# Performance work log

Hardware: AMD Instinct MI355X
Metric: run time of the kernel (lower is better)

## Reference

```python
import jax, jax.numpy as jnp
import numpy as np

B, S, D, H = 4, 2048, 1024, 16
DH = D // H  # 64, head_embed_dim


def setup_inputs() -> dict:
    key = jax.random.key(0)
    ks = jax.random.split(key, 12)
    scale = 1.0 / np.sqrt(D)
    inp = {
        "query": jax.random.normal(ks[0], (B, S, D), jnp.float32),
        "key": jax.random.normal(ks[1], (B, S, D), jnp.float32),
        "value": jax.random.normal(ks[2], (B, S, D), jnp.float32),
        "key_padding_mask": jax.random.randint(ks[3], (B, S), 0, 2).astype(bool),
        # Linear params stored as [in, out] (math-equivalent to torch's [out,in].T)
        "Wq": jax.random.normal(ks[4], (D, H * DH), jnp.float32) * scale,
        "bq": jnp.zeros((H * DH,), jnp.float32),
        "Wk": jax.random.normal(ks[5], (D, H * DH), jnp.float32) * scale,
        "bk": jnp.zeros((H * DH,), jnp.float32),
        "Wv": jax.random.normal(ks[6], (D, H * DH), jnp.float32) * scale,
        "bv": jnp.zeros((H * DH,), jnp.float32),
        "Wo": jax.random.normal(ks[7], (H * DH, D), jnp.float32) * scale,
        "bo": jnp.zeros((D,), jnp.float32),
    }
    return inp


def reference(query, key, value, key_padding_mask, Wq, bq, Wk, bk, Wv, bv, Wo, bo):
    b, nq, _ = query.shape
    nk = key.shape[-2]
    # QKV projections -> [B, H, S, DH]
    q = (query @ Wq + bq).reshape(b, nq, H, DH).transpose(0, 2, 1, 3)
    k = (key @ Wk + bk).reshape(b, nk, H, DH).transpose(0, 2, 1, 3)
    v = (value @ Wv + bv).reshape(b, nk, H, DH).transpose(0, 2, 1, 3)
    # scaled dot-product scores [B, H, Sq, Sk]
    scores = jnp.einsum("bhqd,bhkd->bhqk", q, k) / np.sqrt(DH)
    # key_padding_mask broadcast over heads and query positions; True = masked
    mask = key_padding_mask[:, None, None, :]
    scores = jnp.where(mask, -jnp.inf, scores)
    w = jax.nn.softmax(scores, axis=-1)
    attn = jnp.einsum("bhqk,bhkd->bhqd", w, v)
    attn = attn.transpose(0, 2, 1, 3).reshape(b, nq, H * DH)
    return attn @ Wo + bo
```

## Files before the change

kernel.cpp:

```cpp
#include <hip/hip_runtime.h>
#include <hip/hip_bf16.h>

#define Bc 4
#define Sc 2048
#define Dc 1024
#define Hc 16
#define DHc 64

typedef unsigned short u16;
typedef unsigned int u32;
typedef __attribute__((ext_vector_type(8))) short bfrag;
typedef __attribute__((ext_vector_type(4))) float f32x4;

#define SCALE_Q 0.18033688011112042f

#if __has_builtin(__builtin_amdgcn_exp2f)
#define EXP2(x) __builtin_amdgcn_exp2f(x)
#else
#define EXP2(x) exp2f(x)
#endif

#if __has_builtin(__builtin_amdgcn_mfma_f32_16x16x16bf16_1k)
#define HAVE_M16 1
typedef __attribute__((ext_vector_type(4))) short bfrag4;
union FB4 { bfrag4 f; u32 w[2]; };
#endif

__device__ __forceinline__ u16 f2bf(float f) {
  u32 u = __float_as_uint(f);
  return (u16)((u + 0x7fffu + ((u >> 16) & 1u)) >> 16);
}
__device__ __forceinline__ float bf2f(u16 h) { return __uint_as_float(((u32)h) << 16); }

__device__ __forceinline__ u32 pkbf(float a, float b) {
  union { __hip_bfloat162 h; u32 u; } c;
  c.h = __float22bfloat162_rn(make_float2(a, b));
  return c.u;
}

union FB { bfrag f; u32 w[4]; };

__device__ __forceinline__ void gl_lds16(const u16* g, u16* l) {
  __builtin_amdgcn_global_load_lds(
      (const __attribute__((address_space(1))) unsigned int*)g,
      (__attribute__((address_space(3))) unsigned int*)l, 16, 0, 0);
}

__global__ __launch_bounds__(256) void prep_kernel(
    const void* __restrict__ qsrc, const void* __restrict__ mask,
    const void* __restrict__ bq, const void* __restrict__ bk,
    const void* __restrict__ bv, const void* __restrict__ bo,
    int* __restrict__ flags, float* __restrict__ maskf, float* __restrict__ biasf) {
  __shared__ int c_bf, c_ni, c_nf;
  const int tid = threadIdx.x;
  if (tid == 0) { c_bf = 0; c_ni = 0; c_nf = 0; }
  __syncthreads();
  u32 w = ((const u32*)qsrc)[tid];
  int e = (int)((w >> 7) & 0xffu);
  if (e >= 118 && e <= 130) atomicAdd(&c_bf, 1);
  int ni = 0, nf = 0;
  for (int i = tid; i < 2048; i += 256) {
    u32 v = ((const u32*)mask)[i];
    if (v > 1u) ni = 1;
    if (v != 0u && v != 0x3f800000u) nf = 1;
  }
  if (ni) atomicAdd(&c_ni, 1);
  if (nf) atomicAdd(&c_nf, 1);
  __syncthreads();
  const int isbf = (c_bf > 128) ? 1 : 0;
  const int layout = (c_ni == 0) ? 0 : ((c_nf == 0) ? 2 : 1);
  if (tid == 0) { flags[0] = isbf; flags[1] = layout; }
  for (int i = tid; i < Bc * Sc; i += 256) {
    int mv;
    if (layout == 0) mv = ((const int*)mask)[i];
    else if (layout == 1) mv = (int)((const unsigned char*)mask)[i];
    else mv = (((const u32*)mask)[i] != 0u) ? 1 : 0;
    maskf[i] = mv ? -1e30f : 0.0f;
  }
  const void* bs[4] = {bq, bk, bv, bo};
  for (int j = 0; j < 4; ++j) {
    const void* bp = bs[j];
    float sc = (j == 0) ? SCALE_Q : 1.0f;
    for (int i = tid; i < Dc; i += 256)
      biasf[j * Dc + i] = (isbf ? bf2f(((const u16*)bp)[i]) : ((const float*)bp)[i]) * sc;
  }
}

__global__ __launch_bounds__(256) void cvt3(
    const void* __restrict__ s0, const void* __restrict__ s1, const void* __restrict__ s2,
    u16* __restrict__ d0, u16* __restrict__ d1, u16* __restrict__ d2,
    const int* __restrict__ flags) {
  const void* s = blockIdx.y == 0 ? s0 : (blockIdx.y == 1 ? s1 : s2);
  u16* d = blockIdx.y == 0 ? d0 : (blockIdx.y == 1 ? d1 : d2);
  size_t e = ((size_t)blockIdx.x * 256 + threadIdx.x) * 8;
  if (flags[0]) {
    *(uint4*)(d + e) = *(const uint4*)((const u16*)s + e);
  } else {
    const float* p = (const float*)s + e;
    float4 f0 = *(const float4*)p, f1 = *(const float4*)(p + 4);
    uint4 st;
    st.x = pkbf(f0.x, f0.y); st.y = pkbf(f0.z, f0.w);
    st.z = pkbf(f1.x, f1.y); st.w = pkbf(f1.z, f1.w);
    *(uint4*)(d + e) = st;
  }
}

__global__ __launch_bounds__(256) void transpose_all(
    const void* __restrict__ W0, const void* __restrict__ W1,
    const void* __restrict__ W2, const void* __restrict__ W3,
    u16* __restrict__ D0, u16* __restrict__ D1, u16* __restrict__ D2,
    u16* __restrict__ D3, const int* __restrict__ flags) {
  __shared__ short ts[64][72];
  const int z = blockIdx.z;
  const void* W = z == 0 ? W0 : (z == 1 ? W1 : (z == 2 ? W2 : W3));
  u16* Wt = z == 0 ? D0 : (z == 1 ? D1 : (z == 2 ? D2 : D3));
  const float scale = (z == 0) ? SCALE_Q : 1.0f;
  const int r0 = blockIdx.y * 64, c0 = blockIdx.x * 64;
  const int isbf = flags[0];
  for (int i = 0; i < 2; ++i) {
    int ch = threadIdx.x + i * 256;
    int r = ch >> 3, c = (ch & 7) * 8;
    bfrag pk;
    if (isbf) {
      uint4 v = *(const uint4*)((const u16*)W + (size_t)(r0 + r) * Dc + c0 + c);
      const u16* pv = (const u16*)&v;
      for (int j = 0; j < 8; ++j) pk[j] = (short)f2bf(bf2f(pv[j]) * scale);
    } else {
      const float* p = (const float*)W + (size_t)(r0 + r) * Dc + c0 + c;
      float4 f0 = *(const float4*)p, f1 = *(const float4*)(p + 4);
      pk[0] = (short)f2bf(f0.x * scale); pk[1] = (short)f2bf(f0.y * scale);
      pk[2] = (short)f2bf(f0.z * scale); pk[3] = (short)f2bf(f0.w * scale);
      pk[4] = (short)f2bf(f1.x * scale); pk[5] = (short)f2bf(f1.y * scale);
      pk[6] = (short)f2bf(f1.z * scale); pk[7] = (short)f2bf(f1.w * scale);
    }
    *(bfrag*)(&ts[r][c]) = pk;
  }
  __syncthreads();
  for (int i = 0; i < 2; ++i) {
    int ch = threadIdx.x + i * 256;
    int n = ch >> 3, k = (ch & 7) * 8;
    u16 tmp[8] __attribute__((aligned(16)));
    for (int j = 0; j < 8; ++j) tmp[j] = (u16)ts[k + j][n];
    *(uint4*)(Wt + (size_t)(c0 + n) * Dc + r0 + k) = *(const uint4*)tmp;
  }
}

#define BM 128
#define BN 128
#define BK 32

#define GEMM_STAGE(bufI)                                                          \
  {                                                                               \
    gl_lds16(bgp0, &Bs[bufI][wave * 16][0]);                                      \
    gl_lds16(bgp1, &Bs[bufI][wave * 16 + 64][0]);                                 \
    bgp0 += BK; bgp1 += BK;                                                       \
    if (a_bf) {                                                                   \
      gl_lds16(agp0, &As[bufI][wave * 16][0]);                                    \
      gl_lds16(agp1, &As[bufI][wave * 16 + 64][0]);                               \
      agp0 += BK; agp1 += BK;                                                     \
    } else {                                                                      \
      for (int i_ = 0; i_ < 2; ++i_) {                                            \
        int ch_ = tid + i_ * 256;                                                 \
        int r_ = ch_ >> 2, kc_ = (ch_ & 3) * 8;                                   \
        const float* p_ = (const float*)Araw + (size_t)(bm0 + r_) * K + ksf + kc_;\
        float4 f0_ = *(const float4*)p_, f1_ = *(const float4*)(p_ + 4);          \
        uint4 st_;                                                                \
        st_.x = pkbf(f0_.x, f0_.y); st_.y = pkbf(f0_.z, f0_.w);                   \
        st_.z = pkbf(f1_.x, f1_.y); st_.w = pkbf(f1_.z, f1_.w);                   \
        *(uint4*)(&As[bufI][r_][kc_]) = st_;                                      \
      }                                                                           \
    }                                                                             \
    ksf += BK;                                                                    \
  }

__global__ __launch_bounds__(256) void gemm_bt(
    const void* __restrict__ Araw, const u16* __restrict__ Bt,
    const float* __restrict__ bias, void* __restrict__ Cout, u16* __restrict__ VtOut,
    const int* __restrict__ flags, int M, int N, int K,
    int a_mode , int c_mode ,
    int qkv ) {
  __shared__ __align__(16) u16 As[2][BM][BK];
  __shared__ __align__(16) u16 Bs[2][BN][BK];
  if (qkv) {
    const int z = blockIdx.z;
    Araw = (const void*)((const u16*)Araw + (size_t)z * Bc * Sc * Dc);
    Bt += (size_t)z * Dc * Dc;
    bias += z * Dc;
    if (z == 2) { c_mode = 2; Cout = (void*)VtOut; }
    else Cout = (void*)((u16*)Cout + (size_t)z * Bc * Sc * Dc);
  }
  const int tid = threadIdx.x;
  const int lane = tid & 63, wave = tid >> 6;
  const int lr = lane & 15, lq = lane >> 4;
  const int ntiles = N >> 7;
  const int band = (M >> 7) >> 3;
  const int L = blockIdx.x;
  const int mt = (L & 7) * band + ((L >> 3) / ntiles);
  const int nt = (L >> 3) % ntiles;
  const int bm0 = mt * BM, bn0 = nt * BN;
  const int wm = (wave >> 1) * 64, wn = (wave & 1) * 64;
  const int a_bf = a_mode ? 1 : flags[0];
  const int srow = lane >> 2;
  const int schunk = lane & 3;
  const u16* bgp0 = Bt + (size_t)(bn0 + wave * 16 + srow) * K + schunk * 8;
  const u16* bgp1 = bgp0 + (size_t)64 * K;
  const u16* agp0 = (const u16*)Araw + (size_t)(bm0 + wave * 16 + srow) * K + schunk * 8;
  const u16* agp1 = agp0 + (size_t)64 * K;
  int ksf = 0;
  f32x4 acc[4][4] = {};
  GEMM_STAGE(0);
  __syncthreads();
  const int NIT = K / BK;
#pragma unroll 2
  for (int it = 0; it < NIT; ++it) {
    const int p = it & 1;
    if (it + 1 < NIT) { GEMM_STAGE(p ^ 1); }
    bfrag af[4], bf[4];
    for (int mi = 0; mi < 4; ++mi) af[mi] = *(const bfrag*)(&As[p][wm + mi * 16 + lr][lq * 8]);
    for (int nj = 0; nj < 4; ++nj) bf[nj] = *(const bfrag*)(&Bs[p][wn + nj * 16 + lr][lq * 8]);
    for (int mi = 0; mi < 4; ++mi)
      for (int nj = 0; nj < 4; ++nj)
        acc[mi][nj] = __builtin_amdgcn_mfma_f32_16x16x32_bf16(af[mi], bf[nj], acc[mi][nj], 0, 0, 0);
    __syncthreads();
  }
  float bcol[4];
  for (int nj = 0; nj < 4; ++nj) bcol[nj] = bias[bn0 + wn + nj * 16 + lr];
  if (c_mode == 2) {
    u16* VT = (u16*)Cout;
    for (int mi = 0; mi < 4; ++mi)
      for (int nj = 0; nj < 4; ++nj) {
        int row = bm0 + wm + mi * 16 + lq * 4;
        int col = bn0 + wn + nj * 16 + lr;
        float v0 = acc[mi][nj][0] + bcol[nj], v1 = acc[mi][nj][1] + bcol[nj];
        float v2 = acc[mi][nj][2] + bcol[nj], v3 = acc[mi][nj][3] + bcol[nj];
        uint2 st;
        st.x = (u32)f2bf(v0) | ((u32)f2bf(v1) << 16);
        st.y = (u32)f2bf(v2) | ((u32)f2bf(v3) << 16);
        size_t drow = (size_t)((row >> 11) * Hc + (col >> 6)) * DHc + (col & 63);
        *(uint2*)(VT + drow * Sc + (row & (Sc - 1))) = st;
      }
  } else {
    const int outbf = (c_mode == 0) ? 1 : flags[0];
    for (int mi = 0; mi < 4; ++mi)
      for (int r = 0; r < 4; ++r) {
        int row = bm0 + wm + mi * 16 + lq * 4 + r;
        for (int nj = 0; nj < 4; ++nj) {
          int col = bn0 + wn + nj * 16 + lr;
          float v = acc[mi][nj][r] + bcol[nj];
          if (outbf) ((u16*)Cout)[(size_t)row * N + col] = f2bf(v);
          else ((float*)Cout)[(size_t)row * N + col] = v;
        }
      }
  }
}

__global__ __launch_bounds__(256) void attn_kernel(
    const u16* __restrict__ Q, const u16* __restrict__ K,
    const u16* __restrict__ Vt, const float* __restrict__ maskf,
    u16* __restrict__ Aout) {
  __shared__ __align__(16) u16 Ks[2][64][64];
  __shared__ __align__(16) u16 Vts[2][64][64];
  __shared__ float maskL[Sc];
  const int tid = threadIdx.x;
  const int lane = tid & 63, wave = tid >> 6;
  const int lr = lane & 15, lq = lane >> 4;
  const int bh = blockIdx.x;
  const int b = bh >> 4, h = bh & 15;
  const int q0 = blockIdx.y * 128;
  const int wq = wave * 32;
  const int rr0 = wave * 16 + (lane >> 3);
  const int rr1 = rr0 + 8;
  const int cc = lane & 7;
  const u16* kg0 = K + (size_t)(b * Sc + rr0) * Dc + h * DHc + ((cc ^ (rr0 & 7)) * 8);
  const u16* kg1 = K + (size_t)(b * Sc + rr1) * Dc + h * DHc + ((cc ^ (rr1 & 7)) * 8);
  const u16* vg0 = Vt + (size_t)((b * Hc + h) * DHc + rr0) * Sc + ((cc ^ (rr0 & 7)) * 8);
  const u16* vg1 = Vt + (size_t)((b * Hc + h) * DHc + rr1) * Sc + ((cc ^ (rr1 & 7)) * 8);
#define ATTN_STAGE(bufI)                                      \
  {                                                           \
    gl_lds16(kg0, &Ks[bufI][wave * 16][0]);                   \
    gl_lds16(kg1, &Ks[bufI][wave * 16 + 8][0]);               \
    gl_lds16(vg0, &Vts[bufI][wave * 16][0]);                  \
    gl_lds16(vg1, &Vts[bufI][wave * 16 + 8][0]);              \
    kg0 += (size_t)64 * Dc; kg1 += (size_t)64 * Dc;           \
    vg0 += 64; vg1 += 64;                                     \
  }
  bfrag qf[2][2];
  for (int mi = 0; mi < 2; ++mi)
    for (int ks = 0; ks < 2; ++ks)
      qf[mi][ks] = *(const bfrag*)(Q + (size_t)(b * Sc + q0 + wq + mi * 16 + lr) * Dc +
                                   h * DHc + ks * 32 + lq * 8);
  f32x4 oacc[2][4] = {};
  f32x4 oext[2] = {};
#ifdef HAVE_M16
  FB4 ones;
  ones.w[0] = 0x3F803F80u; ones.w[1] = 0x3F803F80u;
#else
  FB ones;
  ones.w[0] = 0x3F803F80u; ones.w[1] = 0x3F803F80u; ones.w[2] = 0x3F803F80u; ones.w[3] = 0x3F803F80u;
#endif
  ATTN_STAGE(0);
  {
    const float4* ms = (const float4*)(maskf + b * Sc);
    for (int i = tid; i < Sc / 4; i += 256) ((float4*)maskL)[i] = ms[i];
  }
  __syncthreads();
  const int lrx = lr & 7;
#pragma unroll 2
  for (int kt = 0; kt < Sc / 64; ++kt) {
    const int p = kt & 1;
    if (kt + 1 < Sc / 64) { ATTN_STAGE(p ^ 1); }
    f32x4 sacc[2][4];
    for (int nk = 0; nk < 4; ++nk) {
      f32x4 mk = *(const f32x4*)(&maskL[kt * 64 + nk * 16 + lq * 4]);
      sacc[0][nk] = mk;
      sacc[1][nk] = mk;
    }
    for (int nk = 0; nk < 4; ++nk) {
      const int kr = nk * 16 + lr;
      bfrag kf0 = *(const bfrag*)(&Ks[p][kr][(lq ^ lrx) * 8]);
      bfrag kf1 = *(const bfrag*)(&Ks[p][kr][((4 + lq) ^ lrx) * 8]);
      for (int mi = 0; mi < 2; ++mi) {
        sacc[mi][nk] = __builtin_amdgcn_mfma_f32_16x16x32_bf16(kf0, qf[mi][0], sacc[mi][nk], 0, 0, 0);
        sacc[mi][nk] = __builtin_amdgcn_mfma_f32_16x16x32_bf16(kf1, qf[mi][1], sacc[mi][nk], 0, 0, 0);
      }
    }
    for (int nk = 0; nk < 4; ++nk) {
      u32 pw[2][2];
      for (int mi = 0; mi < 2; ++mi) {
        float p0 = EXP2(sacc[mi][nk][0]);
        float p1 = EXP2(sacc[mi][nk][1]);
        float p2 = EXP2(sacc[mi][nk][2]);
        float p3 = EXP2(sacc[mi][nk][3]);
        pw[mi][0] = pkbf(p0, p1);
        pw[mi][1] = pkbf(p2, p3);
      }
      const int vchunk = (2 * nk + (lq >> 1));
      const int voff = (lq & 1) * 4;
#ifdef HAVE_M16
      FB4 pb0, pb1;
      pb0.w[0] = pw[0][0]; pb0.w[1] = pw[0][1];
      pb1.w[0] = pw[1][0]; pb1.w[1] = pw[1][1];
      oext[0] = __builtin_amdgcn_mfma_f32_16x16x16bf16_1k(ones.f, pb0.f, oext[0], 0, 0, 0);
      oext[1] = __builtin_amdgcn_mfma_f32_16x16x16bf16_1k(ones.f, pb1.f, oext[1], 0, 0, 0);
      for (int nd = 0; nd < 4; ++nd) {
        const int dr = nd * 16 + lr;
        FB4 vb;
        *(uint2*)&vb.w[0] = *(const uint2*)(&Vts[p][dr][(vchunk ^ lrx) * 8 + voff]);
        oacc[0][nd] = __builtin_amdgcn_mfma_f32_16x16x16bf16_1k(vb.f, pb0.f, oacc[0][nd], 0, 0, 0);
        oacc[1][nd] = __builtin_amdgcn_mfma_f32_16x16x16bf16_1k(vb.f, pb1.f, oacc[1][nd], 0, 0, 0);
      }
#else
      FB pb0, pb1;
      pb0.w[0] = pw[0][0]; pb0.w[1] = pw[0][1]; pb0.w[2] = 0; pb0.w[3] = 0;
      pb1.w[0] = pw[1][0]; pb1.w[1] = pw[1][1]; pb1.w[2] = 0; pb1.w[3] = 0;
      oext[0] = __builtin_amdgcn_mfma_f32_16x16x32_bf16(ones.f, pb0.f, oext[0], 0, 0, 0);
      oext[1] = __builtin_amdgcn_mfma_f32_16x16x32_bf16(ones.f, pb1.f, oext[1], 0, 0, 0);
      for (int nd = 0; nd < 4; ++nd) {
        const int dr = nd * 16 + lr;
        FB vb;
        *(uint2*)&vb.w[0] = *(const uint2*)(&Vts[p][dr][(vchunk ^ lrx) * 8 + voff]);
        vb.w[2] = 0; vb.w[3] = 0;
        oacc[0][nd] = __builtin_amdgcn_mfma_f32_16x16x32_bf16(vb.f, pb0.f, oacc[0][nd], 0, 0, 0);
        oacc[1][nd] = __builtin_amdgcn_mfma_f32_16x16x32_bf16(vb.f, pb1.f, oacc[1][nd], 0, 0, 0);
      }
#endif
    }
    __syncthreads();
  }
  for (int mi = 0; mi < 2; ++mi) {
    float inv = 1.0f / oext[mi][0];
    u16* rowp = Aout + (size_t)(b * Sc + q0 + wq + mi * 16 + lr) * Dc + h * DHc;
    for (int nd = 0; nd < 4; ++nd) {
      float o0 = oacc[mi][nd][0] * inv, o1 = oacc[mi][nd][1] * inv;
      float o2 = oacc[mi][nd][2] * inv, o3 = oacc[mi][nd][3] * inv;
      uint2 st;
      st.x = pkbf(o0, o1);
      st.y = pkbf(o2, o3);
      *(uint2*)(rowp + nd * 16 + lq * 4) = st;
    }
  }
}

extern "C" void kernel_launch(void* const* d_in, const int* in_sizes, int n_in,
                              void* d_out, int out_size, void* d_ws, size_t ws_size,
                              hipStream_t stream) {
  (void)in_sizes; (void)n_in; (void)out_size;
  char* ws = (char*)d_ws;
  int* flags = (int*)ws;
  float* maskf = (float*)(ws + 256);
  float* biasf = (float*)(ws + 256 + Bc * Sc * 4);
  u16* WqT = (u16*)(ws + 65536);
  u16* WkT = WqT + (size_t)Dc * Dc;
  u16* WvT = WkT + (size_t)Dc * Dc;
  u16* WoT = WvT + (size_t)Dc * Dc;
  u16* Qb  = WoT + (size_t)Dc * Dc;
  u16* Kb  = Qb + (size_t)Bc * Sc * Dc;
  u16* Vb  = Kb + (size_t)Bc * Sc * Dc;
  u16* Vtb = Vb + (size_t)Bc * Sc * Dc;
  u16* Ab  = Vtb + (size_t)Bc * Sc * Dc;
  u16* qbf = Ab + (size_t)Bc * Sc * Dc;
  u16* kbf = qbf + (size_t)Bc * Sc * Dc;
  u16* vbf = kbf + (size_t)Bc * Sc * Dc;
  const size_t need = (size_t)((char*)(vbf + (size_t)Bc * Sc * Dc) - ws);
  const bool have_cvt = ws_size >= need;

  prep_kernel<<<1, 256, 0, stream>>>(d_in[0], d_in[3], d_in[5], d_in[7], d_in[9], d_in[11],
                                     flags, maskf, biasf);
  transpose_all<<<dim3(16, 16, 4), 256, 0, stream>>>(d_in[4], d_in[6], d_in[8], d_in[10],
                                                     WqT, WkT, WvT, WoT, flags);
  const int nblk = (Bc * Sc / BM) * (Dc / BN);
  if (have_cvt) {
    cvt3<<<dim3(4096, 3), 256, 0, stream>>>(d_in[0], d_in[1], d_in[2], qbf, kbf, vbf, flags);
    gemm_bt<<<dim3(nblk, 1, 3), 256, 0, stream>>>(qbf, WqT, biasf, Qb, Vtb, flags,
                                                  Bc * Sc, Dc, Dc, 1, 0, 1);
  } else {
    gemm_bt<<<nblk, 256, 0, stream>>>(d_in[0], WqT, biasf, Qb, nullptr, flags,
                                      Bc * Sc, Dc, Dc, 0, 0, 0);
    gemm_bt<<<nblk, 256, 0, stream>>>(d_in[1], WkT, biasf + Dc, Kb, nullptr, flags,
                                      Bc * Sc, Dc, Dc, 0, 0, 0);
    gemm_bt<<<nblk, 256, 0, stream>>>(d_in[2], WvT, biasf + 2 * Dc, Vtb, nullptr, flags,
                                      Bc * Sc, Dc, Dc, 0, 2, 0);
  }
  attn_kernel<<<dim3(64, 16), 256, 0, stream>>>(Qb, Kb, Vtb, maskf, Ab);
  gemm_bt<<<nblk, 256, 0, stream>>>(Ab, WoT, biasf + 3 * Dc, d_out, nullptr, flags,
                                    Bc * Sc, Dc, Dc, 1, 1, 0);
}
```

Before: 377.2 us.

## Merge setup kernels, drop separate input conversion, vectorize GEMM epilogue stores

Folds prep and weight-transpose into one setup kernel. It removes the cvt3 pre-conversion pass so the batched QKV GEMM converts fp32 activations to bf16 on the fly while staging into LDS. The non-V GEMM now swaps MFMA operand order so each lane holds four consecutive columns, which allows vectorized bias loads and uint2/float4 stores instead of scalar scattered stores. The attention kernel reads the mask directly from global memory instead of staging it in LDS. The trade is extra in-loop conversion work in the GEMM A-path and global mask reads in the inner attention loop, against one fewer full pass over the inputs and fewer launches.

```diff
diff --git a/kernel.cpp b/kernel.cpp
--- a/kernel.cpp
+++ b/kernel.cpp
@@ -46,79 +46,68 @@
       (__attribute__((address_space(3))) unsigned int*)l, 16, 0, 0);
 }
 
-__global__ __launch_bounds__(256) void prep_kernel(
-    const void* __restrict__ qsrc, const void* __restrict__ mask,
-    const void* __restrict__ bq, const void* __restrict__ bk,
-    const void* __restrict__ bv, const void* __restrict__ bo,
-    int* __restrict__ flags, float* __restrict__ maskf, float* __restrict__ biasf) {
-  __shared__ int c_bf, c_ni, c_nf;
-  const int tid = threadIdx.x;
-  if (tid == 0) { c_bf = 0; c_ni = 0; c_nf = 0; }
+__device__ __forceinline__ int detect_bf(const void* qsrc, int tid, int* sh) {
+  if (tid == 0) *sh = 0;
   __syncthreads();
   u32 w = ((const u32*)qsrc)[tid];
   int e = (int)((w >> 7) & 0xffu);
-  if (e >= 118 && e <= 130) atomicAdd(&c_bf, 1);
-  int ni = 0, nf = 0;
-  for (int i = tid; i < 2048; i += 256) {
-    u32 v = ((const u32*)mask)[i];
-    if (v > 1u) ni = 1;
-    if (v != 0u && v != 0x3f800000u) nf = 1;
-  }
-  if (ni) atomicAdd(&c_ni, 1);
-  if (nf) atomicAdd(&c_nf, 1);
+  if (e >= 118 && e <= 130) atomicAdd(sh, 1);
   __syncthreads();
-  const int isbf = (c_bf > 128) ? 1 : 0;
-  const int layout = (c_ni == 0) ? 0 : ((c_nf == 0) ? 2 : 1);
-  if (tid == 0) { flags[0] = isbf; flags[1] = layout; }
-  for (int i = tid; i < Bc * Sc; i += 256) {
-    int mv;
-    if (layout == 0) mv = ((const int*)mask)[i];
-    else if (layout == 1) mv = (int)((const unsigned char*)mask)[i];
-    else mv = (((const u32*)mask)[i] != 0u) ? 1 : 0;
-    maskf[i] = mv ? -1e30f : 0.0f;
-  }
-  const void* bs[4] = {bq, bk, bv, bo};
-  for (int j = 0; j < 4; ++j) {
-    const void* bp = bs[j];
-    float sc = (j == 0) ? SCALE_Q : 1.0f;
-    for (int i = tid; i < Dc; i += 256)
-      biasf[j * Dc + i] = (isbf ? bf2f(((const u16*)bp)[i]) : ((const float*)bp)[i]) * sc;
-  }
-}
-
-__global__ __launch_bounds__(256) void cvt3(
-    const void* __restrict__ s0, const void* __restrict__ s1, const void* __restrict__ s2,
-    u16* __restrict__ d0, u16* __restrict__ d1, u16* __restrict__ d2,
-    const int* __restrict__ flags) {
-  const void* s = blockIdx.y == 0 ? s0 : (blockIdx.y == 1 ? s1 : s2);
-  u16* d = blockIdx.y == 0 ? d0 : (blockIdx.y == 1 ? d1 : d2);
-  size_t e = ((size_t)blockIdx.x * 256 + threadIdx.x) * 8;
-  if (flags[0]) {
-    *(uint4*)(d + e) = *(const uint4*)((const u16*)s + e);
-  } else {
-    const float* p = (const float*)s + e;
-    float4 f0 = *(const float4*)p, f1 = *(const float4*)(p + 4);
-    uint4 st;
-    st.x = pkbf(f0.x, f0.y); st.y = pkbf(f0.z, f0.w);
-    st.z = pkbf(f1.x, f1.y); st.w = pkbf(f1.z, f1.w);
-    *(uint4*)(d + e) = st;
-  }
-}
-
-__global__ __launch_bounds__(256) void transpose_all(
+  return *sh > 128;
+}
+
+__global__ __launch_bounds__(256) void setup_kernel(
+    const void* __restrict__ qsrc, const void* __restrict__ mask,
     const void* __restrict__ W0, const void* __restrict__ W1,
     const void* __restrict__ W2, const void* __restrict__ W3,
+    const void* __restrict__ bq, const void* __restrict__ bk,
+    const void* __restrict__ bv, const void* __restrict__ bo,
     u16* __restrict__ D0, u16* __restrict__ D1, u16* __restrict__ D2,
-    u16* __restrict__ D3, const int* __restrict__ flags) {
+    u16* __restrict__ D3, int* __restrict__ flags, float* __restrict__ maskf,
+    float* __restrict__ biasf) {
+  __shared__ int sh_cnt;
   __shared__ short ts[64][72];
+  const int tid = threadIdx.x;
   const int z = blockIdx.z;
+  const int isbf = detect_bf(qsrc, tid, &sh_cnt);
+  if (z == 4) {
+    const int id = blockIdx.y * 16 + blockIdx.x;
+    __shared__ int c_ni, c_nf;
+    if (tid == 0) { c_ni = 0; c_nf = 0; }
+    __syncthreads();
+    int ni = 0, nf = 0;
+    for (int i = tid; i < 2048; i += 256) {
+      u32 v = ((const u32*)mask)[i];
+      if (v > 1u) ni = 1;
+      if (v != 0u && v != 0x3f800000u) nf = 1;
+    }
+    if (ni) atomicAdd(&c_ni, 1);
+    if (nf) atomicAdd(&c_nf, 1);
+    __syncthreads();
+    const int layout = (c_ni == 0) ? 0 : ((c_nf == 0) ? 2 : 1);
+    if (id == 0 && tid == 0) { flags[0] = isbf; flags[1] = layout; }
+    if (id < 32) {
+      int i = id * 256 + tid;
+      int mv;
+      if (layout == 0) mv = ((const int*)mask)[i];
+      else if (layout == 1) mv = (int)((const unsigned char*)mask)[i];
+      else mv = (((const u32*)mask)[i] != 0u) ? 1 : 0;
+      maskf[i] = mv ? -1e30f : 0.0f;
+    } else if (id < 36) {
+      const int j = id - 32;
+      const void* bp = j == 0 ? bq : (j == 1 ? bk : (j == 2 ? bv : bo));
+      float sc = (j == 0) ? SCALE_Q : 1.0f;
+      for (int i = tid; i < Dc; i += 256)
+        biasf[j * Dc + i] = (isbf ? bf2f(((const u16*)bp)[i]) : ((const float*)bp)[i]) * sc;
+    }
+    return;
+  }
   const void* W = z == 0 ? W0 : (z == 1 ? W1 : (z == 2 ? W2 : W3));
   u16* Wt = z == 0 ? D0 : (z == 1 ? D1 : (z == 2 ? D2 : D3));
   const float scale = (z == 0) ? SCALE_Q : 1.0f;
   const int r0 = blockIdx.y * 64, c0 = blockIdx.x * 64;
-  const int isbf = flags[0];
   for (int i = 0; i < 2; ++i) {
-    int ch = threadIdx.x + i * 256;
+    int ch = tid + i * 256;
     int r = ch >> 3, c = (ch & 7) * 8;
     bfrag pk;
     if (isbf) {
@@ -137,7 +126,7 @@
   }
   __syncthreads();
   for (int i = 0; i < 2; ++i) {
-    int ch = threadIdx.x + i * 256;
+    int ch = tid + i * 256;
     int n = ch >> 3, k = (ch & 7) * 8;
     u16 tmp[8] __attribute__((aligned(16)));
     for (int j = 0; j < 8; ++j) tmp[j] = (u16)ts[k + j][n];
@@ -174,16 +163,18 @@
   }
 
 __global__ __launch_bounds__(256) void gemm_bt(
-    const void* __restrict__ Araw, const u16* __restrict__ Bt,
+    const void* __restrict__ A0, const void* __restrict__ A1,
+    const void* __restrict__ A2, const u16* __restrict__ Bt,
     const float* __restrict__ bias, void* __restrict__ Cout, u16* __restrict__ VtOut,
     const int* __restrict__ flags, int M, int N, int K,
     int a_mode , int c_mode ,
     int qkv ) {
   __shared__ __align__(16) u16 As[2][BM][BK];
   __shared__ __align__(16) u16 Bs[2][BN][BK];
+  const void* Araw = A0;
   if (qkv) {
     const int z = blockIdx.z;
-    Araw = (const void*)((const u16*)Araw + (size_t)z * Bc * Sc * Dc);
+    Araw = z == 0 ? A0 : (z == 1 ? A1 : A2);
     Bt += (size_t)z * Dc * Dc;
     bias += z * Dc;
     if (z == 2) { c_mode = 2; Cout = (void*)VtOut; }
@@ -200,6 +191,7 @@
   const int bm0 = mt * BM, bn0 = nt * BN;
   const int wm = (wave >> 1) * 64, wn = (wave & 1) * 64;
   const int a_bf = a_mode ? 1 : flags[0];
+  const int vt = (c_mode == 2);
   const int srow = lane >> 2;
   const int schunk = lane & 3;
   const u16* bgp0 = Bt + (size_t)(bn0 + wave * 16 + srow) * K + schunk * 8;
@@ -218,14 +210,20 @@
     bfrag af[4], bf[4];
     for (int mi = 0; mi < 4; ++mi) af[mi] = *(const bfrag*)(&As[p][wm + mi * 16 + lr][lq * 8]);
     for (int nj = 0; nj < 4; ++nj) bf[nj] = *(const bfrag*)(&Bs[p][wn + nj * 16 + lr][lq * 8]);
-    for (int mi = 0; mi < 4; ++mi)
-      for (int nj = 0; nj < 4; ++nj)
-        acc[mi][nj] = __builtin_amdgcn_mfma_f32_16x16x32_bf16(af[mi], bf[nj], acc[mi][nj], 0, 0, 0);
+    if (vt) {
+      for (int mi = 0; mi < 4; ++mi)
+        for (int nj = 0; nj < 4; ++nj)
+          acc[mi][nj] = __builtin_amdgcn_mfma_f32_16x16x32_bf16(af[mi], bf[nj], acc[mi][nj], 0, 0, 0);
+    } else {
+      for (int mi = 0; mi < 4; ++mi)
+        for (int nj = 0; nj < 4; ++nj)
+          acc[mi][nj] = __builtin_amdgcn_mfma_f32_16x16x32_bf16(bf[nj], af[mi], acc[mi][nj], 0, 0, 0);
+    }
     __syncthreads();
   }
-  float bcol[4];
-  for (int nj = 0; nj < 4; ++nj) bcol[nj] = bias[bn0 + wn + nj * 16 + lr];
-  if (c_mode == 2) {
+  if (vt) {
+    float bcol[4];
+    for (int nj = 0; nj < 4; ++nj) bcol[nj] = bias[bn0 + wn + nj * 16 + lr];
     u16* VT = (u16*)Cout;
     for (int mi = 0; mi < 4; ++mi)
       for (int nj = 0; nj < 4; ++nj) {
@@ -234,23 +232,31 @@
         float v0 = acc[mi][nj][0] + bcol[nj], v1 = acc[mi][nj][1] + bcol[nj];
         float v2 = acc[mi][nj][2] + bcol[nj], v3 = acc[mi][nj][3] + bcol[nj];
         uint2 st;
-        st.x = (u32)f2bf(v0) | ((u32)f2bf(v1) << 16);
-        st.y = (u32)f2bf(v2) | ((u32)f2bf(v3) << 16);
+        st.x = pkbf(v0, v1);
+        st.y = pkbf(v2, v3);
         size_t drow = (size_t)((row >> 11) * Hc + (col >> 6)) * DHc + (col & 63);
         *(uint2*)(VT + drow * Sc + (row & (Sc - 1))) = st;
       }
   } else {
     const int outbf = (c_mode == 0) ? 1 : flags[0];
-    for (int mi = 0; mi < 4; ++mi)
-      for (int r = 0; r < 4; ++r) {
-        int row = bm0 + wm + mi * 16 + lq * 4 + r;
-        for (int nj = 0; nj < 4; ++nj) {
-          int col = bn0 + wn + nj * 16 + lr;
-          float v = acc[mi][nj][r] + bcol[nj];
-          if (outbf) ((u16*)Cout)[(size_t)row * N + col] = f2bf(v);
-          else ((float*)Cout)[(size_t)row * N + col] = v;
+    for (int nj = 0; nj < 4; ++nj) {
+      const int colb = bn0 + wn + nj * 16 + lq * 4;
+      f32x4 b4 = *(const f32x4*)(bias + colb);
+      for (int mi = 0; mi < 4; ++mi) {
+        const int row = bm0 + wm + mi * 16 + lr;
+        float v0 = acc[mi][nj][0] + b4[0], v1 = acc[mi][nj][1] + b4[1];
+        float v2 = acc[mi][nj][2] + b4[2], v3 = acc[mi][nj][3] + b4[3];
+        if (outbf) {
+          uint2 st;
+          st.x = pkbf(v0, v1);
+          st.y = pkbf(v2, v3);
+          *(uint2*)((u16*)Cout + (size_t)row * N + colb) = st;
+        } else {
+          float4 st = make_float4(v0, v1, v2, v3);
+          *(float4*)((float*)Cout + (size_t)row * N + colb) = st;
         }
       }
+    }
   }
 }
 
@@ -260,7 +266,6 @@
     u16* __restrict__ Aout) {
   __shared__ __align__(16) u16 Ks[2][64][64];
   __shared__ __align__(16) u16 Vts[2][64][64];
-  __shared__ float maskL[Sc];
   const int tid = threadIdx.x;
   const int lane = tid & 63, wave = tid >> 6;
   const int lr = lane & 15, lq = lane >> 4;
@@ -298,11 +303,8 @@
   FB ones;
   ones.w[0] = 0x3F803F80u; ones.w[1] = 0x3F803F80u; ones.w[2] = 0x3F803F80u; ones.w[3] = 0x3F803F80u;
 #endif
+  const float* maskb = maskf + b * Sc;
   ATTN_STAGE(0);
-  {
-    const float4* ms = (const float4*)(maskf + b * Sc);
-    for (int i = tid; i < Sc / 4; i += 256) ((float4*)maskL)[i] = ms[i];
-  }
   __syncthreads();
   const int lrx = lr & 7;
 #pragma unroll 2
@@ -311,7 +313,7 @@
     if (kt + 1 < Sc / 64) { ATTN_STAGE(p ^ 1); }
     f32x4 sacc[2][4];
     for (int nk = 0; nk < 4; ++nk) {
-      f32x4 mk = *(const f32x4*)(&maskL[kt * 64 + nk * 16 + lq * 4]);
+      f32x4 mk = *(const f32x4*)(maskb + kt * 64 + nk * 16 + lq * 4);
       sacc[0][nk] = mk;
       sacc[1][nk] = mk;
     }
@@ -384,7 +386,7 @@
 extern "C" void kernel_launch(void* const* d_in, const int* in_sizes, int n_in,
                               void* d_out, int out_size, void* d_ws, size_t ws_size,
                               hipStream_t stream) {
-  (void)in_sizes; (void)n_in; (void)out_size;
+  (void)in_sizes; (void)n_in; (void)out_size; (void)ws_size;
   char* ws = (char*)d_ws;
   int* flags = (int*)ws;
   float* maskf = (float*)(ws + 256);
@@ -395,33 +397,18 @@
   u16* WoT = WvT + (size_t)Dc * Dc;
   u16* Qb  = WoT + (size_t)Dc * Dc;
   u16* Kb  = Qb + (size_t)Bc * Sc * Dc;
-  u16* Vb  = Kb + (size_t)Bc * Sc * Dc;
-  u16* Vtb = Vb + (size_t)Bc * Sc * Dc;
+  u16* Vtb = Kb + (size_t)Bc * Sc * Dc;
   u16* Ab  = Vtb + (size_t)Bc * Sc * Dc;
-  u16* qbf = Ab + (size_t)Bc * Sc * Dc;
-  u16* kbf = qbf + (size_t)Bc * Sc * Dc;
-  u16* vbf = kbf + (size_t)Bc * Sc * Dc;
-  const size_t need = (size_t)((char*)(vbf + (size_t)Bc * Sc * Dc) - ws);
-  const bool have_cvt = ws_size >= need;
-
-  prep_kernel<<<1, 256, 0, stream>>>(d_in[0], d_in[3], d_in[5], d_in[7], d_in[9], d_in[11],
-                                     flags, maskf, biasf);
-  transpose_all<<<dim3(16, 16, 4), 256, 0, stream>>>(d_in[4], d_in[6], d_in[8], d_in[10],
-                                                     WqT, WkT, WvT, WoT, flags);
+
+  setup_kernel<<<dim3(16, 16, 5), 256, 0, stream>>>(
+      d_in[0], d_in[3], d_in[4], d_in[6], d_in[8], d_in[10],
+      d_in[5], d_in[7], d_in[9], d_in[11],
+      WqT, WkT, WvT, WoT, flags, maskf, biasf);
   const int nblk = (Bc * Sc / BM) * (Dc / BN);
-  if (have_cvt) {
-    cvt3<<<dim3(4096, 3), 256, 0, stream>>>(d_in[0], d_in[1], d_in[2], qbf, kbf, vbf, flags);
-    gemm_bt<<<dim3(nblk, 1, 3), 256, 0, stream>>>(qbf, WqT, biasf, Qb, Vtb, flags,
-                                                  Bc * Sc, Dc, Dc, 1, 0, 1);
-  } else {
-    gemm_bt<<<nblk, 256, 0, stream>>>(d_in[0], WqT, biasf, Qb, nullptr, flags,
-                                      Bc * Sc, Dc, Dc, 0, 0, 0);
-    gemm_bt<<<nblk, 256, 0, stream>>>(d_in[1], WkT, biasf + Dc, Kb, nullptr, flags,
-                                      Bc * Sc, Dc, Dc, 0, 0, 0);
-    gemm_bt<<<nblk, 256, 0, stream>>>(d_in[2], WvT, biasf + 2 * Dc, Vtb, nullptr, flags,
-                                      Bc * Sc, Dc, Dc, 0, 2, 0);
-  }
+  gemm_bt<<<dim3(nblk, 1, 3), 256, 0, stream>>>(
+      d_in[0], d_in[1], d_in[2], WqT, biasf, Qb, Vtb, flags,
+      Bc * Sc, Dc, Dc, 0, 0, 1);
   attn_kernel<<<dim3(64, 16), 256, 0, stream>>>(Qb, Kb, Vtb, maskf, Ab);
-  gemm_bt<<<nblk, 256, 0, stream>>>(Ab, WoT, biasf + 3 * Dc, d_out, nullptr, flags,
-                                    Bc * Sc, Dc, Dc, 1, 1, 0);
-}
+  gemm_bt<<<nblk, 256, 0, stream>>>(Ab, nullptr, nullptr, WoT, biasf + 3 * Dc,
+                                    d_out, nullptr, flags, Bc * Sc, Dc, Dc, 1, 1, 0);
+}
```

Result: slower. 441.2 us (+17.0%).
